# Kernel tuning notes

Measured on AMD Instinct MI355X. Metric: run time of the kernel, lower is better.

The kernel has to match this reference:

```python
import jax, jax.numpy as jnp
import numpy as np

B, T, A, H, E = 512, 64, 32, 512, 32


def sinusoidal_pos_encoding(t, dim):
    # t: (B, T) float positions -> (B, T, dim)
    half = dim // 2
    freqs = jnp.exp(-jnp.log(10000.0) * jnp.arange(half, dtype=jnp.float32) / half)
    ang = t[..., None] * freqs  # (B, T, half)
    return jnp.concatenate([jnp.sin(ang), jnp.cos(ang)], axis=-1)


def cat_linear(x, W, b, cat_ids):
    # x: (B, T, Din); W: (E, Din, Dout); b: (E, Dout); cat_ids: (B,)
    Wg = W[cat_ids]            # (B, Din, Dout) gathered per-sample weights
    bg = b[cat_ids][:, None]   # (B, 1, Dout)
    return jnp.einsum('btd,bdh->bth', x, Wg) + bg


def swish(x):
    return x * jax.nn.sigmoid(x)


def setup_inputs() -> dict:
    key = jax.random.key(0)
    ks = jax.random.split(key, 10)
    s = lambda fan_in: 1.0 / np.sqrt(fan_in)
    return {
        'actions': jax.random.normal(ks[0], (B, T, A), dtype=jnp.float32),
        'timesteps': jax.random.uniform(ks[1], (B,), dtype=jnp.float32),
        'cat_ids': jax.random.randint(ks[2], (B,), 0, E),
        'W1': jax.random.normal(ks[3], (E, A, H), dtype=jnp.float32) * s(A),
        'b1': jnp.zeros((E, H), dtype=jnp.float32),
        'W2': jax.random.normal(ks[4], (E, 2 * H, H), dtype=jnp.float32) * s(2 * H),
        'b2': jnp.zeros((E, H), dtype=jnp.float32),
        'W3': jax.random.normal(ks[5], (E, H, H), dtype=jnp.float32) * s(H),
        'b3': jnp.zeros((E, H), dtype=jnp.float32),
    }


def reference(actions, timesteps, cat_ids, W1, b1, W2, b2, W3, b3):
    b, t, _ = actions.shape
    timesteps_bt = jnp.broadcast_to(timesteps[:, None], (b, t))
    a_emb = cat_linear(actions, W1, b1, cat_ids)              # (B, T, H)
    tau_emb = sinusoidal_pos_encoding(timesteps_bt, H).astype(a_emb.dtype)
    x = jnp.concatenate([a_emb, tau_emb], axis=-1)            # (B, T, 2H)
    x = swish(cat_linear(x, W2, b2, cat_ids))                 # (B, T, H)
    x = cat_linear(x, W3, b3, cat_ids)                        # (B, T, H)
    return x
```

## Files before the change

kernel.cpp:

```cpp
#include <hip/hip_runtime.h>
#include <hip/hip_bf16.h>

#define B_ 512
#define T_ 64
#define A_ 32
#define H_ 512
#define E_ 32
#define MAX_TASKS 272
#define CAP_ 168
#define GRID_ (8 * CAP_)
#define TSC 16

typedef unsigned short u16;
typedef unsigned int u32;
typedef __attribute__((ext_vector_type(8))) short short8;
typedef __attribute__((ext_vector_type(4))) float floatx4;

static __device__ __forceinline__ u16 f2bf(float f) {
    u32 u = __builtin_bit_cast(u32, f);
    u += 0x7fffu + ((u >> 16) & 1u);
    return (u16)(u >> 16);
}

static __device__ __forceinline__ void gl2lds16(const u16* g, u16* l) {
    __builtin_amdgcn_global_load_lds(
        (const __attribute__((address_space(1))) void*)g,
        (__attribute__((address_space(3))) void*)l, 16, 0, 0);
}

__global__ void group_kernel(const int* __restrict__ cat_ids,
                             int* __restrict__ sample_list,
                             int4* __restrict__ tasks,
                             int* __restrict__ itemlist,
                             int* __restrict__ eoff_g,
                             int* __restrict__ ecnt_g) {
    __shared__ int cnt[E_], off[E_], cur[E_], toff[E_], jc[8];
    __shared__ int total, fb;
    int tid = threadIdx.x;
    if (tid < E_) { cnt[tid] = 0; cur[tid] = 0; }
    __syncthreads();
    int e = cat_ids[tid];
    atomicAdd(&cnt[e], 1);
    __syncthreads();
    if (tid == 0) {
        int run = 0, trun = 0;
        for (int i = 0; i < E_; i++) {
            off[i] = run;  run += cnt[i];
            toff[i] = trun; trun += (cnt[i] + 1) >> 1;
        }
        total = trun;
    }
    __syncthreads();
    if (tid < E_) {
        int c = cnt[tid], o = off[tid], to = toff[tid];
        eoff_g[tid] = o;
        ecnt_g[tid] = c;
        for (int j = 0; j < c; j += 2)
            tasks[to++] = make_int4(tid, o + j, (c - j >= 2) ? 2 : 1, 0);
    }
    if (tid < 8) {
        int J = 0;
        for (int cc = 0; cc < 4; cc++) J += 4 * ((cnt[tid + 8 * cc] + 1) >> 1);
        jc[tid] = J;
    }
    __syncthreads();
    if (tid == 0) {
        int f = 0;
        for (int x = 0; x < 8; x++) if (jc[x] > CAP_) f = 1;
        fb = f;
    }
    __syncthreads();
    if (!fb) {
        if (tid < 8) {
            int j = 0;
            for (int cc = 0; cc < 4; cc++) {
                int ee = tid + 8 * cc;
                int nt = (cnt[ee] + 1) >> 1, t0 = toff[ee];
                for (int t = t0; t < t0 + nt; t++)
                    for (int nb = 0; nb < 4; nb++) {
                        itemlist[tid + 8 * j] = (t << 2) | nb;
                        j++;
                    }
            }
            for (; j < CAP_; j++) itemlist[tid + 8 * j] = -1;
        }
    } else {
        for (int f = tid; f < GRID_; f += 512)
            itemlist[f] = (f < 4 * total) ? f : -1;
    }
    int p = atomicAdd(&cur[e], 1);
    sample_list[off[e] + p] = tid;
}

__global__ __launch_bounds__(256) void embed_kernel(
        const float* __restrict__ actions, const float* __restrict__ timesteps,
        const int* __restrict__ cat_ids, const float* __restrict__ W1,
        const float* __restrict__ b1, u16* __restrict__ a_emb,
        float* __restrict__ tauG) {
    int b = blockIdx.x;
    int tid = threadIdx.x;
    int e = cat_ids[b];

    {
        float tval = timesteps[b];
        float freq = expf(-9.210340371976184f * (float)tid * (1.0f / 256.0f));
        float ang = tval * freq;
        tauG[(size_t)b * H_ + tid]       = sinf(ang);
        tauG[(size_t)b * H_ + 256 + tid] = cosf(ang);
    }

    __shared__ float act[T_ * A_];
    const float* asrc = actions + (size_t)b * T_ * A_;
    for (int i = tid; i < T_ * A_; i += 256) act[i] = asrc[i];
    __syncthreads();

    const float* w1 = W1 + (size_t)e * A_ * H_;
    int n0 = tid, n1 = tid + 256;
    float wA[A_], wB[A_];
#pragma unroll
    for (int k = 0; k < A_; k++) {
        wA[k] = w1[k * H_ + n0];
        wB[k] = w1[k * H_ + n1];
    }
    float bA = b1[e * H_ + n0], bB = b1[e * H_ + n1];
    u16* orow = a_emb + (size_t)b * T_ * H_;
    for (int tt = 0; tt < T_; tt++) {
        float accA = bA, accB = bB;
#pragma unroll
        for (int k = 0; k < A_; k++) {
            float a = act[tt * A_ + k];
            accA = fmaf(a, wA[k], accA);
            accB = fmaf(a, wB[k], accB);
        }
        orow[tt * H_ + n0] = f2bf(accA);
        orow[tt * H_ + n1] = f2bf(accB);
    }
}

__global__ __launch_bounds__(256) void convert_transpose(
        const float* __restrict__ W, u16* __restrict__ Wt, int srcK, int dstK) {
    int n = blockIdx.y * 256 + threadIdx.x;
    int k0 = blockIdx.x * 32;
    int e = blockIdx.z;
    const float* src = W + ((size_t)e * srcK + k0) * H_ + n;
    short8 out[4];
#pragma unroll
    for (int j = 0; j < 32; j++)
        out[j >> 3][j & 7] = (short)f2bf(src[(size_t)j * H_]);
    u16* dst = Wt + ((size_t)e * H_ + n) * dstK + k0;
#pragma unroll
    for (int c = 0; c < 4; c++) *(short8*)(dst + c * 8) = out[c];
}

__global__ __launch_bounds__(256) void tau_bias_kernel(
        const float* __restrict__ W2, const float* __restrict__ b2,
        const float* __restrict__ tauG, const int* __restrict__ sample_list,
        const int* __restrict__ eoff, const int* __restrict__ ecnt,
        float* __restrict__ bias2s) {
    int cc = blockIdx.x;
    int e = blockIdx.y;
    int cnt = ecnt[e], off = eoff[e];
    if (cnt == 0) return;
    int tid = threadIdx.x;
    int k8 = tid >> 5, ln = tid & 31;
    int wv = tid >> 6;
    int n0 = cc * 64 + ln, n1 = n0 + 32;
    const float* wb = W2 + ((size_t)e * 1024 + 512) * H_;

    __shared__ float tauT[512][20];
    __shared__ float pS[4][TSC][64];

    for (int c0 = 0; c0 < cnt; c0 += TSC) {
        for (int i = tid; i < TSC * 512; i += 256) {
            int sl = i >> 9, k = i & 511;
            float v = 0.f;
            if (c0 + sl < cnt)
                v = tauG[(size_t)sample_list[off + c0 + sl] * H_ + k];
            tauT[k][sl] = v;
        }
        __syncthreads();

        float a0[TSC], a1[TSC];
#pragma unroll
        for (int s = 0; s < TSC; s++) { a0[s] = 0.f; a1[s] = 0.f; }

#pragma unroll 8
        for (int j = 0; j < 64; j++) {
            int k = k8 + j * 8;
            float w0 = wb[(size_t)k * H_ + n0];
            float w1 = wb[(size_t)k * H_ + n1];
            float tv[TSC];
            *(float4*)&tv[0]  = *(const float4*)&tauT[k][0];
            *(float4*)&tv[4]  = *(const float4*)&tauT[k][4];
            *(float4*)&tv[8]  = *(const float4*)&tauT[k][8];
            *(float4*)&tv[12] = *(const float4*)&tauT[k][12];
#pragma unroll
            for (int s = 0; s < TSC; s++) {
                a0[s] = fmaf(tv[s], w0, a0[s]);
                a1[s] = fmaf(tv[s], w1, a1[s]);
            }
        }

#pragma unroll
        for (int s = 0; s < TSC; s++) {
            a0[s] += __shfl_xor(a0[s], 32, 64);
            a1[s] += __shfl_xor(a1[s], 32, 64);
        }
        if (!(tid & 32)) {
#pragma unroll
            for (int s = 0; s < TSC; s++) {
                pS[wv][s][ln]      = a0[s];
                pS[wv][s][ln + 32] = a1[s];
            }
        }
        __syncthreads();

        for (int o = tid; o < TSC * 64; o += 256) {
            int sl = o >> 6, l = o & 63;
            if (c0 + sl < cnt) {
                float v = pS[0][sl][l] + pS[1][sl][l] +
                          pS[2][sl][l] + pS[3][sl][l];
                int s = sample_list[off + c0 + sl];
                int col = cc * 64 + l;
                bias2s[(size_t)s * H_ + col] = v + b2[e * H_ + col];
            }
        }
        __syncthreads();
    }
}

template <int DIN, bool PSBIAS, bool DO_SWISH, bool OUT_BF16>
__global__ __launch_bounds__(256, 2) void moe_gemm(
        const u16* __restrict__ xsrc, const u16* __restrict__ Wt,
        const float* __restrict__ bias,
        const int* __restrict__ sample_list, const int4* __restrict__ tasks,
        const int* __restrict__ itemlist, void* __restrict__ outp) {
    int item = itemlist[blockIdx.x];
    if (item < 0) return;
    int4 task = tasks[item >> 2];
    int nb = item & 3;
    int ns = task.z;
    int e = task.x;
    int s0 = sample_list[task.y];
    int s1 = (ns > 1) ? sample_list[task.y + 1] : s0;
    int n0 = nb * 128;

    int tid = threadIdx.x;
    int lane = tid & 63, wv = tid >> 6;
    int wr = wv >> 1, wc = wv & 1;
    int quad = lane >> 4, c15 = lane & 15;
    int r8 = lane >> 3, cg = lane & 7;

    __shared__ __align__(16) u16 xs[2][128 * 64];
    __shared__ __align__(16) u16 wt[2][128 * 64];

    floatx4 acc[4][4];
    floatx4 zero4 = {0.f, 0.f, 0.f, 0.f};
#pragma unroll
    for (int i = 0; i < 4; i++)
#pragma unroll
        for (int j = 0; j < 4; j++) acc[i][j] = zero4;

    const u16* wbase = Wt + (size_t)(e * H_ + n0) * DIN;
    int kc_sw = (cg ^ r8) * 8;

    auto stage = [&](int b, int k0) {
#pragma unroll
        for (int h = 0; h < 4; h++) {
            int rbase = h * 32 + wv * 8;
            int s = (h < 2) ? s0 : s1;
            int t = (rbase + r8) & 63;
            gl2lds16(xsrc + ((size_t)s * T_ + t) * H_ + k0 + kc_sw,
                     &xs[b][rbase * 64]);
        }
#pragma unroll
        for (int h = 0; h < 4; h++) {
            int nbase = h * 32 + wv * 8;
            gl2lds16(wbase + (size_t)(nbase + r8) * DIN + k0 + kc_sw,
                     &wt[b][nbase * 64]);
        }
    };

    auto compute = [&](int b) {
#pragma unroll
        for (int kk = 0; kk < 2; kk++) {
            int c = kk * 4 + quad;
            short8 af[4], bfr[4];
#pragma unroll
            for (int i = 0; i < 4; i++) {
                int row = wr * 64 + i * 16 + c15;
                af[i] = *(const short8*)&xs[b][row * 64 + ((c ^ (row & 7)) * 8)];
                int nr = wc * 64 + i * 16 + c15;
                bfr[i] = *(const short8*)&wt[b][nr * 64 + ((c ^ (nr & 7)) * 8)];
            }
#pragma unroll
            for (int mt = 0; mt < 4; mt++)
#pragma unroll
                for (int nt = 0; nt < 4; nt++)
                    acc[mt][nt] = __builtin_amdgcn_mfma_f32_16x16x32_bf16(
                            af[mt], bfr[nt], acc[mt][nt], 0, 0, 0);
        }
    };

    constexpr int KI = DIN / 64;
    stage(0, 0);
    __syncthreads();
#pragma unroll
    for (int t = 0; t < KI; ++t) {
        if (t + 1 < KI) stage((t + 1) & 1, (t + 1) * 64);
        compute(t & 1);
        if (t + 1 < KI) __syncthreads();
    }

    if (wr >= ns) return;
    int s = (wr == 0) ? s0 : s1;
    const float* bp = PSBIAS ? (bias + (size_t)s * H_)
                             : (bias + (size_t)e * H_);
#pragma unroll
    for (int mt = 0; mt < 4; mt++) {
        int tb = mt * 16 + quad * 4;
#pragma unroll
        for (int nt = 0; nt < 4; nt++) {
            int col = n0 + wc * 64 + nt * 16 + c15;
            float bv = bp[col];
#pragma unroll
            for (int r = 0; r < 4; r++) {
                float v = acc[mt][nt][r] + bv;
                if (DO_SWISH) v = v / (1.0f + expf(-v));
                size_t oidx = ((size_t)s * T_ + tb + r) * H_ + col;
                if (OUT_BF16) ((u16*)outp)[oidx] = f2bf(v);
                else          ((float*)outp)[oidx] = v;
            }
        }
    }
}

extern "C" void kernel_launch(void* const* d_in, const int* in_sizes, int n_in,
                              void* d_out, int out_size, void* d_ws, size_t ws_size,
                              hipStream_t stream) {
    const float* actions   = (const float*)d_in[0];
    const float* timesteps = (const float*)d_in[1];
    const int*   cat_ids   = (const int*)d_in[2];
    const float* W1 = (const float*)d_in[3];
    const float* b1 = (const float*)d_in[4];
    const float* W2 = (const float*)d_in[5];
    const float* b2 = (const float*)d_in[6];
    const float* W3 = (const float*)d_in[7];
    const float* b3 = (const float*)d_in[8];

    char* ws = (char*)d_ws;
    u16* a_emb = (u16*)ws;
    u16* y     = (u16*)(ws + (size_t)32 * 1024 * 1024);
    char* meta = ws + (size_t)64 * 1024 * 1024 + 512 * 1024;
    int*  sample_list = (int*)meta;
    int4* tasks       = (int4*)(meta + 8192);
    int*  itemlist    = (int*)(meta + 16384);
    int*  eoff        = (int*)(meta + 24576);
    int*  ecnt        = (int*)(meta + 24576 + 128);
    u16*  Wt2a   = (u16*)d_out;
    float* bias2s = (float*)((char*)d_out + (size_t)48 * 1024 * 1024);
    float* tauG   = (float*)((char*)d_out + (size_t)52 * 1024 * 1024);
    u16*  Wt3    = a_emb;

    hipLaunchKernelGGL(group_kernel, dim3(1), dim3(512), 0, stream,
                       cat_ids, sample_list, tasks, itemlist, eoff, ecnt);
    hipLaunchKernelGGL(embed_kernel, dim3(512), dim3(256), 0, stream,
                       actions, timesteps, cat_ids, W1, b1, a_emb, tauG);
    hipLaunchKernelGGL(convert_transpose, dim3(H_ / 32, 2, E_), dim3(256),
                       0, stream, W2, Wt2a, 2 * H_, H_);
    hipLaunchKernelGGL(tau_bias_kernel, dim3(8, E_), dim3(256), 0, stream,
                       W2, b2, tauG, sample_list, eoff, ecnt, bias2s);
    hipLaunchKernelGGL((moe_gemm<H_, true, true, true>), dim3(GRID_),
                       dim3(256), 0, stream,
                       a_emb, Wt2a, bias2s, sample_list, tasks, itemlist,
                       (void*)y);
    hipLaunchKernelGGL(convert_transpose, dim3(H_ / 32, 2, E_), dim3(256),
                       0, stream, W3, Wt3, H_, H_);
    hipLaunchKernelGGL((moe_gemm<H_, false, false, false>), dim3(GRID_),
                       dim3(256), 0, stream,
                       y, Wt3, b3, sample_list, tasks, itemlist, d_out);
}
```

Before: 318.6 us.

## Split tau-bias K dimension across blocks with atomic accumulation; widen transpose tiles

The tau-projection bias kernel now splits the 512-long K reduction into four 128-chunks across a third grid dimension, giving four times as many blocks. Partial sums are combined with atomic float adds into bias2s, which the embed kernel pre-initializes with b2. Each thread now handles one output column instead of two. Separately, the weight convert/transpose kernel processes 64 K rows per thread instead of 32, halving its block count. The changes add atomic traffic and make the summation order nondeterministic in exchange for more parallelism in a previously underfilled kernel.

```diff
diff --git a/kernel.cpp b/kernel.cpp
--- a/kernel.cpp
+++ b/kernel.cpp
@@ -95,8 +95,9 @@
 __global__ __launch_bounds__(256) void embed_kernel(
         const float* __restrict__ actions, const float* __restrict__ timesteps,
         const int* __restrict__ cat_ids, const float* __restrict__ W1,
-        const float* __restrict__ b1, u16* __restrict__ a_emb,
-        float* __restrict__ tauG) {
+        const float* __restrict__ b1, const float* __restrict__ b2,
+        u16* __restrict__ a_emb, float* __restrict__ tauG,
+        float* __restrict__ bias2s) {
     int b = blockIdx.x;
     int tid = threadIdx.x;
     int e = cat_ids[b];
@@ -107,6 +108,8 @@
         float ang = tval * freq;
         tauG[(size_t)b * H_ + tid]       = sinf(ang);
         tauG[(size_t)b * H_ + 256 + tid] = cosf(ang);
+        bias2s[(size_t)b * H_ + tid]       = b2[e * H_ + tid];
+        bias2s[(size_t)b * H_ + 256 + tid] = b2[e * H_ + 256 + tid];
     }
 
     __shared__ float act[T_ * A_];
@@ -140,79 +143,66 @@
 __global__ __launch_bounds__(256) void convert_transpose(
         const float* __restrict__ W, u16* __restrict__ Wt, int srcK, int dstK) {
     int n = blockIdx.y * 256 + threadIdx.x;
-    int k0 = blockIdx.x * 32;
+    int k0 = blockIdx.x * 64;
     int e = blockIdx.z;
     const float* src = W + ((size_t)e * srcK + k0) * H_ + n;
-    short8 out[4];
-#pragma unroll
-    for (int j = 0; j < 32; j++)
+    short8 out[8];
+#pragma unroll
+    for (int j = 0; j < 64; j++)
         out[j >> 3][j & 7] = (short)f2bf(src[(size_t)j * H_]);
     u16* dst = Wt + ((size_t)e * H_ + n) * dstK + k0;
 #pragma unroll
-    for (int c = 0; c < 4; c++) *(short8*)(dst + c * 8) = out[c];
+    for (int c = 0; c < 8; c++) *(short8*)(dst + c * 8) = out[c];
 }
 
 __global__ __launch_bounds__(256) void tau_bias_kernel(
-        const float* __restrict__ W2, const float* __restrict__ b2,
-        const float* __restrict__ tauG, const int* __restrict__ sample_list,
+        const float* __restrict__ W2, const float* __restrict__ tauG,
+        const int* __restrict__ sample_list,
         const int* __restrict__ eoff, const int* __restrict__ ecnt,
         float* __restrict__ bias2s) {
     int cc = blockIdx.x;
-    int e = blockIdx.y;
+    int e  = blockIdx.y;
+    int kq = blockIdx.z;
     int cnt = ecnt[e], off = eoff[e];
     if (cnt == 0) return;
     int tid = threadIdx.x;
-    int k8 = tid >> 5, ln = tid & 31;
-    int wv = tid >> 6;
-    int n0 = cc * 64 + ln, n1 = n0 + 32;
-    const float* wb = W2 + ((size_t)e * 1024 + 512) * H_;
-
-    __shared__ float tauT[512][20];
+    int ks = tid >> 6;
+    int ln = tid & 63;
+    int n = cc * 64 + ln;
+    const float* wb = W2 + ((size_t)e * 1024 + 512 + kq * 128) * H_;
+
+    __shared__ float tauT[128][20];
     __shared__ float pS[4][TSC][64];
 
     for (int c0 = 0; c0 < cnt; c0 += TSC) {
-        for (int i = tid; i < TSC * 512; i += 256) {
-            int sl = i >> 9, k = i & 511;
+        for (int i = tid; i < TSC * 128; i += 256) {
+            int sl = i >> 7, k = i & 127;
             float v = 0.f;
             if (c0 + sl < cnt)
-                v = tauG[(size_t)sample_list[off + c0 + sl] * H_ + k];
+                v = tauG[(size_t)sample_list[off + c0 + sl] * H_ + kq * 128 + k];
             tauT[k][sl] = v;
         }
         __syncthreads();
 
-        float a0[TSC], a1[TSC];
-#pragma unroll
-        for (int s = 0; s < TSC; s++) { a0[s] = 0.f; a1[s] = 0.f; }
+        float a[TSC];
+#pragma unroll
+        for (int s = 0; s < TSC; s++) a[s] = 0.f;
 
 #pragma unroll 8
-        for (int j = 0; j < 64; j++) {
-            int k = k8 + j * 8;
-            float w0 = wb[(size_t)k * H_ + n0];
-            float w1 = wb[(size_t)k * H_ + n1];
+        for (int j = 0; j < 32; j++) {
+            int k = ks * 32 + j;
+            float w = wb[(size_t)k * H_ + n];
             float tv[TSC];
             *(float4*)&tv[0]  = *(const float4*)&tauT[k][0];
             *(float4*)&tv[4]  = *(const float4*)&tauT[k][4];
             *(float4*)&tv[8]  = *(const float4*)&tauT[k][8];
             *(float4*)&tv[12] = *(const float4*)&tauT[k][12];
 #pragma unroll
-            for (int s = 0; s < TSC; s++) {
-                a0[s] = fmaf(tv[s], w0, a0[s]);
-                a1[s] = fmaf(tv[s], w1, a1[s]);
-            }
-        }
-
-#pragma unroll
-        for (int s = 0; s < TSC; s++) {
-            a0[s] += __shfl_xor(a0[s], 32, 64);
-            a1[s] += __shfl_xor(a1[s], 32, 64);
-        }
-        if (!(tid & 32)) {
-#pragma unroll
-            for (int s = 0; s < TSC; s++) {
-                pS[wv][s][ln]      = a0[s];
-                pS[wv][s][ln + 32] = a1[s];
-            }
-        }
+            for (int s = 0; s < TSC; s++) a[s] = fmaf(tv[s], w, a[s]);
+        }
+
+#pragma unroll
+        for (int s = 0; s < TSC; s++) pS[ks][s][ln] = a[s];
         __syncthreads();
 
         for (int o = tid; o < TSC * 64; o += 256) {
@@ -221,8 +211,7 @@
                 float v = pS[0][sl][l] + pS[1][sl][l] +
                           pS[2][sl][l] + pS[3][sl][l];
                 int s = sample_list[off + c0 + sl];
-                int col = cc * 64 + l;
-                bias2s[(size_t)s * H_ + col] = v + b2[e * H_ + col];
+                unsafeAtomicAdd(&bias2s[(size_t)s * H_ + cc * 64 + l], v);
             }
         }
         __syncthreads();
@@ -365,16 +354,17 @@
     hipLaunchKernelGGL(group_kernel, dim3(1), dim3(512), 0, stream,
                        cat_ids, sample_list, tasks, itemlist, eoff, ecnt);
     hipLaunchKernelGGL(embed_kernel, dim3(512), dim3(256), 0, stream,
-                       actions, timesteps, cat_ids, W1, b1, a_emb, tauG);
-    hipLaunchKernelGGL(convert_transpose, dim3(H_ / 32, 2, E_), dim3(256),
+                       actions, timesteps, cat_ids, W1, b1, b2, a_emb, tauG,
+                       bias2s);
+    hipLaunchKernelGGL(convert_transpose, dim3(H_ / 64, 2, E_), dim3(256),
                        0, stream, W2, Wt2a, 2 * H_, H_);
-    hipLaunchKernelGGL(tau_bias_kernel, dim3(8, E_), dim3(256), 0, stream,
-                       W2, b2, tauG, sample_list, eoff, ecnt, bias2s);
+    hipLaunchKernelGGL(tau_bias_kernel, dim3(8, E_, 4), dim3(256), 0, stream,
+                       W2, tauG, sample_list, eoff, ecnt, bias2s);
     hipLaunchKernelGGL((moe_gemm<H_, true, true, true>), dim3(GRID_),
                        dim3(256), 0, stream,
                        a_emb, Wt2a, bias2s, sample_list, tasks, itemlist,
                        (void*)y);
-    hipLaunchKernelGGL(convert_transpose, dim3(H_ / 32, 2, E_), dim3(256),
+    hipLaunchKernelGGL(convert_transpose, dim3(H_ / 64, 2, E_), dim3(256),
                        0, stream, W3, Wt3, H_, H_);
     hipLaunchKernelGGL((moe_gemm<H_, false, false, false>), dim3(GRID_),
                        dim3(256), 0, stream,
```

Measured after the change: 303.3 us. 4.8% less time.
